# Performance work log

Hardware: AMD Instinct MI355X
Metric: run time of the kernel (lower is better)

The kernel has to match this reference:

```python
import jax, jax.numpy as jnp
import numpy as np

EMBED_DIM = 2048
N_HEADS = 32
N_GROUPS = 8
HEAD_SIZE = EMBED_DIM // N_HEADS  # 64
SCALE = HEAD_SIZE ** -0.5
B, S = 2, 2048


def setup_inputs() -> dict:
    key = jax.random.key(0)
    ks = jax.random.split(key, 7)
    kv_dim = N_GROUPS * HEAD_SIZE
    x = jax.random.normal(ks[0], (B, S, EMBED_DIM), dtype=jnp.float32)
    # Linear weights stored [in, out] (y = x @ W), matching torch nn.Linear math.
    Wq = jax.random.normal(ks[1], (EMBED_DIM, EMBED_DIM), dtype=jnp.float32) * (EMBED_DIM ** -0.5)
    Wk = jax.random.normal(ks[2], (EMBED_DIM, kv_dim), dtype=jnp.float32) * (EMBED_DIM ** -0.5)
    Wv = jax.random.normal(ks[3], (EMBED_DIM, kv_dim), dtype=jnp.float32) * (EMBED_DIM ** -0.5)
    Wo = jax.random.normal(ks[4], (EMBED_DIM, EMBED_DIM), dtype=jnp.float32) * (EMBED_DIM ** -0.5)
    bo = jnp.zeros((EMBED_DIM,), dtype=jnp.float32)
    # causal boolean mask [S, S], broadcast over batch and heads
    mask = jnp.tril(jnp.ones((S, S), dtype=jnp.bool_))
    return {"x": x, "Wq": Wq, "Wk": Wk, "Wv": Wv, "Wo": Wo, "bo": bo, "mask": mask}


def reference(x, Wq, Wk, Wv, Wo, bo, mask):
    B_, S_, E = x.shape
    q = (x @ Wq).reshape(B_, S_, N_HEADS, HEAD_SIZE).transpose(0, 2, 1, 3)   # [B,H,S,D]
    k = (x @ Wk).reshape(B_, S_, N_GROUPS, HEAD_SIZE).transpose(0, 2, 1, 3)  # [B,G,S,D]
    v = (x @ Wv).reshape(B_, S_, N_GROUPS, HEAD_SIZE).transpose(0, 2, 1, 3)
    # GQA: each KV head serves H//G consecutive query heads (matches torch expand+reshape)
    rep = N_HEADS // N_GROUPS
    k = jnp.repeat(k, rep, axis=1)  # [B,H,S,D]
    v = jnp.repeat(v, rep, axis=1)
    scores = SCALE * jnp.einsum("bhqd,bhkd->bhqk", q, k)          # [B,H,S,S]
    scores = jnp.where(mask, scores, -jnp.inf)
    weights = jax.nn.softmax(scores, axis=-1)                      # dropout in eval mode (identity)
    attn = jnp.einsum("bhqk,bhkd->bhqd", weights, v)               # [B,H,S,D]
    attn = attn.transpose(0, 2, 1, 3).reshape(B_, S_, E)
    return attn @ Wo + bo
```

## Files before the change

kernel.cpp:

```cpp
#include <hip/hip_runtime.h>
#include <hip/hip_fp16.h>

#define E_DIM 2048
#define S_LEN 2048
#define NH 32
#define HD 64
#define KV_DIM 512
#define QKV_N 3072
#define M_ROWS 4096
#define QK_SCALE 0.18033688011112042f

typedef __bf16 bf16x8 __attribute__((ext_vector_type(8)));
typedef float f32x4 __attribute__((ext_vector_type(4)));

__device__ __forceinline__ void async_lds16(const __bf16* g, __bf16* l) {
    __builtin_amdgcn_global_load_lds(
        (const __attribute__((address_space(1))) void*)g,
        (__attribute__((address_space(3))) void*)l, 16, 0, 0);
}

#define BAR() asm volatile("s_barrier" ::: "memory")

__global__ void k_convert(const float* __restrict__ x, __bf16* __restrict__ xb, int n) {
    int i = (blockIdx.x * blockDim.x + threadIdx.x) * 4;
    if (i < n) {
        float4 v = *(const float4*)(x + i);
        xb[i + 0] = (__bf16)v.x;
        xb[i + 1] = (__bf16)v.y;
        xb[i + 2] = (__bf16)v.z;
        xb[i + 3] = (__bf16)v.w;
    }
}

__global__ void k_transpose_all(const float* __restrict__ Wq, const float* __restrict__ Wk,
                                const float* __restrict__ Wv, const float* __restrict__ Wo,
                                __bf16* __restrict__ WtAll, __bf16* __restrict__ WoT) {
    const int which = blockIdx.z;
    const float* W;
    __bf16* dst;
    int N;
    float scale = 1.f;
    if (which == 0)      { W = Wq; dst = WtAll;                                    N = E_DIM;  scale = QK_SCALE; }
    else if (which == 1) { W = Wk; dst = WtAll + (size_t)E_DIM * E_DIM;            N = KV_DIM; }
    else if (which == 2) { W = Wv; dst = WtAll + (size_t)(E_DIM + KV_DIM) * E_DIM; N = KV_DIM; }
    else                 { W = Wo; dst = WoT;                                      N = E_DIM;  }
    const int n0 = blockIdx.x * 32;
    if (n0 >= N) return;
    const int k0 = blockIdx.y * 32;
    __shared__ float tile[32][33];
    int tx = threadIdx.x, ty = threadIdx.y;
#pragma unroll
    for (int j = 0; j < 4; ++j)
        tile[ty + j * 8][tx] = W[(size_t)(k0 + ty + j * 8) * N + n0 + tx];
    __syncthreads();
#pragma unroll
    for (int j = 0; j < 4; ++j)
        dst[(size_t)(n0 + ty + j * 8) * E_DIM + k0 + tx] = (__bf16)(tile[tx][ty + j * 8] * scale);
}

#define STG(g, l, bb, hh, kt) do {                                                              \
    async_lds16((g) + (size_t)((hh) * 128) * K + (size_t)(kt) * 64,                             \
                (l) + (bb) * 16384 + (hh) * 8192);                                              \
    async_lds16((g) + (size_t)((hh) * 128 + 64) * K + (size_t)(kt) * 64,                        \
                (l) + (bb) * 16384 + (hh) * 8192 + 4096);                                       \
} while (0)

#define LDA_(p, mq) do {                                                                        \
    _Pragma("unroll") for (int i_ = 0; i_ < 4; ++i_) {                                          \
        const char* rp_ = pAs + (p) * 32768 + ((mq) * 128 + rA + i_ * 16) * 128;                \
        a[i_][0] = *(const bf16x8*)(rp_ + swzk0);                                               \
        a[i_][1] = *(const bf16x8*)(rp_ + swzk1);                                               \
    }                                                                                           \
} while (0)

#define LDB_(p, nq, b) do {                                                                     \
    _Pragma("unroll") for (int j_ = 0; j_ < 2; ++j_) {                                          \
        const char* rp_ = pBs + (p) * 32768 + ((nq) * 128 + rB + j_ * 16) * 128;                \
        b[j_][0] = *(const bf16x8*)(rp_ + swzk0);                                               \
        b[j_][1] = *(const bf16x8*)(rp_ + swzk1);                                               \
    }                                                                                           \
} while (0)

#define MM(mq, nq, b) do {                                                                      \
    __builtin_amdgcn_s_setprio(1);                                                              \
    _Pragma("unroll") for (int i_ = 0; i_ < 4; ++i_)                                            \
    _Pragma("unroll") for (int j_ = 0; j_ < 2; ++j_) {                                          \
        acc[mq][nq][i_][j_] = __builtin_amdgcn_mfma_f32_16x16x32_bf16(                          \
            a[i_][0], b[j_][0], acc[mq][nq][i_][j_], 0, 0, 0);                                  \
        acc[mq][nq][i_][j_] = __builtin_amdgcn_mfma_f32_16x16x32_bf16(                          \
            a[i_][1], b[j_][1], acc[mq][nq][i_][j_], 0, 0, 0);                                  \
    }                                                                                           \
    __builtin_amdgcn_s_setprio(0);                                                              \
} while (0)

#define GROUP(p, kt, S1, S2, WAITSTMT) do {                                                     \
    LDA_(p, 0);                                                                                 \
    LDB_(p, 0, b0);                                                                             \
    if (S1) STG(gA, lA, (p) ^ 1, 1, (kt) + 1);                                                  \
    BAR(); MM(0, 0, b0); BAR();                                                                 \
    LDB_(p, 1, b1);                                                                             \
    if (S2) STG(gA, lA, (p), 0, (kt) + 2);                                                      \
    BAR(); MM(0, 1, b1); BAR();                                                                 \
    LDA_(p, 1);                                                                                 \
    if (S2) STG(gB, lB, (p), 0, (kt) + 2);                                                      \
    BAR(); MM(1, 1, b1); BAR();                                                                 \
    if (S2) STG(gB, lB, (p), 1, (kt) + 2);                                                      \
    WAITSTMT;                                                                                   \
    BAR(); MM(1, 0, b0); BAR();                                                                 \
} while (0)

__global__ __launch_bounds__(512, 2)
void k_gemm8(const __bf16* __restrict__ A, const __bf16* __restrict__ Bt,
             __bf16* __restrict__ C, int M, int N, int K) {
    __shared__ __attribute__((aligned(16))) __bf16 As[2][16384];
    __shared__ __attribute__((aligned(16))) __bf16 Bs[2][16384];
    const int T = K >> 6;
    const int nbx = N >> 8;
    const int bid = blockIdx.x;
    const int swz = (bid & 7) * ((int)gridDim.x >> 3) + (bid >> 3);
    const int m0 = (swz / nbx) << 8;
    const int n0 = (swz % nbx) << 8;

    const int t = threadIdx.x;
    const int lane = t & 63, w = t >> 6;
    const int quad = lane >> 4, l16 = lane & 15;
    const int wr = w >> 2, wc = w & 3;

    const int rbase = w * 8 + (lane >> 3);
    const int cswz = ((lane & 7) ^ (lane >> 3)) * 8;
    const __bf16* gA = A + (size_t)(m0 + rbase) * K + cswz;
    const __bf16* gB = Bt + (size_t)(n0 + rbase) * K + cswz;
    __bf16* lA = &As[0][0] + w * 512;
    __bf16* lB = &Bs[0][0] + w * 512;

    const int swzk0 = ((0 + quad) ^ (l16 & 7)) * 16;
    const int swzk1 = ((4 + quad) ^ (l16 & 7)) * 16;
    const int rA = wr * 64 + l16;
    const int rB = wc * 32 + l16;
    const char* pAs = (const char*)&As[0][0];
    const char* pBs = (const char*)&Bs[0][0];

    f32x4 acc[2][2][4][2] = {};
    bf16x8 a[4][2], b0[2][2], b1[2][2];

    STG(gA, lA, 0, 0, 0); STG(gA, lA, 0, 1, 0);
    STG(gB, lB, 0, 0, 0); STG(gB, lB, 0, 1, 0);
    STG(gA, lA, 1, 0, 1);
    STG(gB, lB, 1, 0, 1); STG(gB, lB, 1, 1, 1);
    asm volatile("s_waitcnt vmcnt(6)" ::: "memory");
    BAR();

    int p = 0;
    for (int kt = 0; kt < T - 2; ++kt) {
        GROUP(p, kt, 1, 1, asm volatile("s_waitcnt vmcnt(6)" ::: "memory"));
        p ^= 1;
    }
    GROUP(p, T - 2, 1, 0, asm volatile("s_waitcnt vmcnt(0)" ::: "memory"));
    p ^= 1;
    GROUP(p, T - 1, 0, 0, (void)0);

#pragma unroll
    for (int mq = 0; mq < 2; ++mq)
#pragma unroll
        for (int nq = 0; nq < 2; ++nq)
#pragma unroll
            for (int i = 0; i < 4; ++i)
#pragma unroll
                for (int j = 0; j < 2; ++j) {
                    const int row = m0 + mq * 128 + wr * 64 + i * 16 + quad * 4;
                    const int col = n0 + nq * 128 + wc * 32 + j * 16 + l16;
#pragma unroll
                    for (int r = 0; r < 4; ++r)
                        C[(size_t)(row + r) * N + col] = (__bf16)acc[mq][nq][i][j][r];
                }
    (void)M;
}

#define STGA_O(bb, kt) do {                                                                     \
    async_lds16(gA + (size_t)(kt) * 64,                  &As[bb][0] + w * 512);                  \
    async_lds16(gA + (size_t)64 * K + (size_t)(kt) * 64, &As[bb][0] + 4096 + w * 512);          \
} while (0)
#define STGB_O(bb, kt, hh) do {                                                                 \
    async_lds16(gB + (size_t)((hh) * 128) * K + (size_t)(kt) * 64,                              \
                &Bs[bb][0] + (hh) * 8192 + w * 512);                                            \
    async_lds16(gB + (size_t)((hh) * 128 + 64) * K + (size_t)(kt) * 64,                         \
                &Bs[bb][0] + (hh) * 8192 + 4096 + w * 512);                                     \
} while (0)

#define LDA_O(p, mq) do {                                                                       \
    _Pragma("unroll") for (int i_ = 0; i_ < 2; ++i_) {                                          \
        const char* rp_ = pAs + (p) * 16384 + ((mq) * 32 + rA + i_ * 16) * 128;                 \
        a[i_][0] = *(const bf16x8*)(rp_ + swzk0);                                               \
        a[i_][1] = *(const bf16x8*)(rp_ + swzk1);                                               \
    }                                                                                           \
} while (0)

#define LDB_O(p, nq, b) do {                                                                    \
    _Pragma("unroll") for (int j_ = 0; j_ < 2; ++j_) {                                          \
        const char* rp_ = pBs + (p) * 32768 + ((nq) * 128 + rB + j_ * 16) * 128;                \
        b[j_][0] = *(const bf16x8*)(rp_ + swzk0);                                               \
        b[j_][1] = *(const bf16x8*)(rp_ + swzk1);                                               \
    }                                                                                           \
} while (0)

#define MM_O(mq, nq, b) do {                                                                    \
    __builtin_amdgcn_s_setprio(1);                                                              \
    _Pragma("unroll") for (int i_ = 0; i_ < 2; ++i_)                                            \
    _Pragma("unroll") for (int j_ = 0; j_ < 2; ++j_) {                                          \
        acc[mq][nq][i_][j_] = __builtin_amdgcn_mfma_f32_16x16x32_bf16(                          \
            a[i_][0], b[j_][0], acc[mq][nq][i_][j_], 0, 0, 0);                                  \
        acc[mq][nq][i_][j_] = __builtin_amdgcn_mfma_f32_16x16x32_bf16(                          \
            a[i_][1], b[j_][1], acc[mq][nq][i_][j_], 0, 0, 0);                                  \
    }                                                                                           \
    __builtin_amdgcn_s_setprio(0);                                                              \
} while (0)

#define GROUP_O(p, kt, S1, S2, WAITSTMT) do {                                                   \
    LDA_O(p, 0);                                                                                \
    LDB_O(p, 0, b0);                                                                            \
    if (S1) STGB_O((p) ^ 1, (kt) + 1, 1);                                                       \
    BAR(); MM_O(0, 0, b0); BAR();                                                               \
    LDB_O(p, 1, b1);                                                                            \
    if (S2) STGB_O(p, (kt) + 2, 0);                                                             \
    BAR(); MM_O(0, 1, b1); BAR();                                                               \
    LDA_O(p, 1);                                                                                \
    BAR(); MM_O(1, 1, b1); BAR();                                                               \
    if (S2) STGA_O(p, (kt) + 2);                                                                \
    WAITSTMT;                                                                                   \
    BAR(); MM_O(1, 0, b0); BAR();                                                               \
} while (0)

__global__ __launch_bounds__(512, 2)
void k_gemm8o(const __bf16* __restrict__ A, const __bf16* __restrict__ Bt,
              float* __restrict__ C, const float* __restrict__ bias,
              int M, int N, int K) {
    __shared__ __attribute__((aligned(16))) __bf16 As[2][8192];
    __shared__ __attribute__((aligned(16))) __bf16 Bs[2][16384];
    const int T = K >> 6;
    const int nbx = N >> 8;
    const int bid = blockIdx.x;
    const int swz = (bid & 7) * ((int)gridDim.x >> 3) + (bid >> 3);
    const int m0 = (swz / nbx) << 7;
    const int n0 = (swz % nbx) << 8;

    const int t = threadIdx.x;
    const int lane = t & 63, w = t >> 6;
    const int quad = lane >> 4, l16 = lane & 15;
    const int wr = w >> 2, wc = w & 3;

    const int rbase = w * 8 + (lane >> 3);
    const int cswz = ((lane & 7) ^ (lane >> 3)) * 8;
    const __bf16* gA = A + (size_t)(m0 + rbase) * K + cswz;
    const __bf16* gB = Bt + (size_t)(n0 + rbase) * K + cswz;

    const int swzk0 = ((0 + quad) ^ (l16 & 7)) * 16;
    const int swzk1 = ((4 + quad) ^ (l16 & 7)) * 16;
    const int rA = wr * 64 + l16;
    const int rB = wc * 32 + l16;
    const char* pAs = (const char*)&As[0][0];
    const char* pBs = (const char*)&Bs[0][0];

    f32x4 acc[2][2][2][2] = {};
    bf16x8 a[2][2], b0[2][2], b1[2][2];

    STGA_O(0, 0); STGB_O(0, 0, 0); STGB_O(0, 0, 1);
    STGB_O(1, 1, 0); STGA_O(1, 1);
    asm volatile("s_waitcnt vmcnt(4)" ::: "memory");
    BAR();

    int p = 0;
    for (int kt = 0; kt < T - 2; ++kt) {
        GROUP_O(p, kt, 1, 1, asm volatile("s_waitcnt vmcnt(4)" ::: "memory"));
        p ^= 1;
    }
    GROUP_O(p, T - 2, 1, 0, asm volatile("s_waitcnt vmcnt(0)" ::: "memory"));
    p ^= 1;
    GROUP_O(p, T - 1, 0, 0, (void)0);

#pragma unroll
    for (int mq = 0; mq < 2; ++mq)
#pragma unroll
        for (int nq = 0; nq < 2; ++nq)
#pragma unroll
            for (int i = 0; i < 2; ++i)
#pragma unroll
                for (int j = 0; j < 2; ++j) {
                    const int row = m0 + wr * 64 + mq * 32 + i * 16 + quad * 4;
                    const int col = n0 + nq * 128 + wc * 32 + j * 16 + l16;
#pragma unroll
                    for (int r = 0; r < 4; ++r)
                        C[(size_t)(row + r) * N + col] = acc[mq][nq][i][j][r] + bias[col];
                }
    (void)M;
}

__global__ __launch_bounds__(256, 3)
void k_attn(const __bf16* __restrict__ qkv, __half* __restrict__ partO,
            float* __restrict__ partL) {
    const int xr = (int)(gridDim.x - 1 - blockIdx.x);
    int qi, c;
    if (xr < 8)       { qi = xr;                  c = 0; }
    else if (xr < 24) { qi = 8 + ((xr - 8) >> 1); c = (xr - 8) & 1; }
    else if (xr < 48) { qi = 16 + (xr - 24) / 3;  c = (xr - 24) % 3; }
    else              { qi = 24 + ((xr - 48) >> 2); c = (xr - 48) & 3; }
    const int q0 = qi * 64;
    const int k_lo = c * 512;
    const int k_hi = min(k_lo + 512, q0 + 64);

    const int gp = blockIdx.y;
    const int g = gp >> 1;
    const int h0 = g * 4 + (gp & 1) * 2;
    const int b = blockIdx.z;
    const int t = threadIdx.x;
    const int lane = t & 63, wave = t >> 6;
    const int quad = lane >> 4, l16 = lane & 15;

    __shared__ __attribute__((aligned(16))) __bf16 Kls[128 * 64];
    __shared__ __attribute__((aligned(16))) __bf16 vT[64][136];
    __shared__ __attribute__((aligned(16))) __bf16 pT[4][2][1024];

    const __bf16* base = qkv + (size_t)b * S_LEN * QKV_N;
    const int qrow = q0 + wave * 16 + l16;

    bf16x8 qf[2][2];
#pragma unroll
    for (int h = 0; h < 2; ++h)
#pragma unroll
        for (int s = 0; s < 2; ++s)
            qf[h][s] = *(const bf16x8*)(base + (size_t)qrow * QKV_N + (h0 + h) * HD + s * 32 + quad * 8);

    f32x4 o[2][4] = {};
    float l_st[2] = {0.f, 0.f};

    const int vkey = lane * 2, vdg = wave * 16;
    const __bf16* vsrc = base + (E_DIM + KV_DIM) + g * HD + vdg;
    const __bf16* ksrc = base + E_DIM + g * HD;

    const int klocal = lane >> 3;
    const int kdblk = (lane & 7) ^ (klocal & 7);
    const __bf16* gk_base = ksrc + (size_t)(wave * 32 + klocal) * QKV_N + kdblk * 8;
    __bf16* lk_base = Kls + wave * 2048;

    auto qk = [&](int m, f32x4* sA, f32x4* sB) {
        __builtin_amdgcn_s_setprio(1);
#pragma unroll
        for (int kt = 0; kt < 4; ++kt) {
            const int kr = m * 64 + kt * 16 + l16;
            const char* kb_ = (const char*)Kls + kr * 128;
            bf16x8 kf0 = *(const bf16x8*)(kb_ + ((quad ^ (kr & 7)) * 16));
            bf16x8 kf1 = *(const bf16x8*)(kb_ + (((4 + quad) ^ (kr & 7)) * 16));
            f32x4 z = {};
            z = __builtin_amdgcn_mfma_f32_16x16x32_bf16(kf0, qf[0][0], z, 0, 0, 0);
            sA[kt] = __builtin_amdgcn_mfma_f32_16x16x32_bf16(kf1, qf[0][1], z, 0, 0, 0);
            f32x4 ww = {};
            ww = __builtin_amdgcn_mfma_f32_16x16x32_bf16(kf0, qf[1][0], ww, 0, 0, 0);
            sB[kt] = __builtin_amdgcn_mfma_f32_16x16x32_bf16(kf1, qf[1][1], ww, 0, 0, 0);
        }
        __builtin_amdgcn_s_setprio(0);
    };

    auto softmax_p = [&](int kb, int h, f32x4* sc) {
        const bool diag = (kb == q0);
        char* prow = (char*)&pT[wave][h][0] + l16 * 128;
        float lsum = 0.f;
#pragma unroll
        for (int kt = 0; kt < 4; ++kt) {
            f32x4 pv_;
#pragma unroll
            for (int r = 0; r < 4; ++r) pv_[r] = exp2f(sc[kt][r]);
            if (diag) {
                const int kbase = kb + kt * 16 + quad * 4;
#pragma unroll
                for (int r = 0; r < 4; ++r)
                    if (kbase + r > qrow) pv_[r] = 0.f;
            }
#pragma unroll
            for (int r = 0; r < 4; ++r) lsum += pv_[r];
            __bf16 pb[4];
#pragma unroll
            for (int r = 0; r < 4; ++r) pb[r] = (__bf16)pv_[r];
            *(uint2*)(prow + ((2 * kt + (quad >> 1)) ^ (l16 & 7)) * 16 + (quad & 1) * 8) =
                *(const uint2*)pb;
        }
        l_st[h] += lsum;
    };

    auto pv = [&](int m) {
        bf16x8 vf[4][2];
        const int koff = m * 64;
#pragma unroll
        for (int cc = 0; cc < 4; ++cc)
#pragma unroll
            for (int kh = 0; kh < 2; ++kh)
                vf[cc][kh] = *(const bf16x8*)&vT[cc * 16 + l16][koff + kh * 32 + quad * 8];
        __builtin_amdgcn_s_setprio(1);
#pragma unroll
        for (int h = 0; h < 2; ++h) {
            const char* prow = (const char*)&pT[wave][h][0] + l16 * 128;
            bf16x8 pf0 = *(const bf16x8*)(prow + ((0 + quad) ^ (l16 & 7)) * 16);
            bf16x8 pf1 = *(const bf16x8*)(prow + ((4 + quad) ^ (l16 & 7)) * 16);
#pragma unroll
            for (int cc = 0; cc < 4; ++cc) {
                o[h][cc] = __builtin_amdgcn_mfma_f32_16x16x32_bf16(vf[cc][0], pf0, o[h][cc], 0, 0, 0);
                o[h][cc] = __builtin_amdgcn_mfma_f32_16x16x32_bf16(vf[cc][1], pf1, o[h][cc], 0, 0, 0);
            }
        }
        __builtin_amdgcn_s_setprio(0);
    };

    for (int kv0 = k_lo; kv0 < k_hi; kv0 += 128) {
#pragma unroll
        for (int i = 0; i < 4; ++i)
            async_lds16(gk_base + (size_t)(kv0 + i * 8) * QKV_N, lk_base + i * 512);

        const __bf16* vp = vsrc + (size_t)(kv0 + vkey) * QKV_N;
        uint4 va0 = *(const uint4*)(vp);
        uint4 va1 = *(const uint4*)(vp + 8);
        uint4 vb0 = *(const uint4*)(vp + QKV_N);
        uint4 vb1 = *(const uint4*)(vp + QKV_N + 8);

        {
            const unsigned short* a0 = (const unsigned short*)&va0;
            const unsigned short* a1 = (const unsigned short*)&va1;
            const unsigned short* b0_ = (const unsigned short*)&vb0;
            const unsigned short* b1_ = (const unsigned short*)&vb1;
#pragma unroll
            for (int j = 0; j < 8; ++j) {
                *(uint32_t*)&vT[vdg + j][vkey] = (uint32_t)a0[j] | ((uint32_t)b0_[j] << 16);
                *(uint32_t*)&vT[vdg + 8 + j][vkey] = (uint32_t)a1[j] | ((uint32_t)b1_[j] << 16);
            }
        }
        __syncthreads();

        f32x4 scA[4], scB[4];
        qk(0, scA, scB);
        softmax_p(kv0, 0, scA);
        softmax_p(kv0, 1, scB);
        pv(0);

        const int kb1 = kv0 + 64;
        if (kb1 < k_hi) {
            qk(1, scA, scB);
            softmax_p(kb1, 0, scA);
            softmax_p(kb1, 1, scB);
            pv(1);
        }
        __syncthreads();
    }

    const size_t blk = ((size_t)b * 16 + gp) * 80 + xr;
    const size_t pb = blk * (2 * 64 * 64);
#pragma unroll
    for (int h = 0; h < 2; ++h) {
        float lt = l_st[h];
        lt += __shfl_xor(lt, 16);
        lt += __shfl_xor(lt, 32);
        const float inv = 1.f / lt;
        __half* prowO = partO + pb + (size_t)(h * 64 + wave * 16 + l16) * 64 + quad * 4;
#pragma unroll
        for (int dt = 0; dt < 4; ++dt) {
            __half ob[4];
#pragma unroll
            for (int r = 0; r < 4; ++r) ob[r] = __float2half(o[h][dt][r] * inv);
            *(uint2*)(prowO + dt * 16) = *(const uint2*)ob;
        }
        if (quad == 0)
            partL[blk * 128 + h * 64 + wave * 16 + l16] = lt;
    }
}

__global__ __launch_bounds__(256, 4)
void k_combine(const __half* __restrict__ partO, const float* __restrict__ partL,
               __bf16* __restrict__ attnb) {
    const int qi = blockIdx.x, gp = blockIdx.y, b = blockIdx.z;
    const int nc = (qi >> 3) + 1;
    int x0;
    if (qi < 8) x0 = qi;
    else if (qi < 16) x0 = 8 + (qi - 8) * 2;
    else if (qi < 24) x0 = 24 + (qi - 16) * 3;
    else x0 = 48 + (qi - 24) * 4;

    const int t = threadIdx.x;
    const int row = t >> 1, half = t & 1;
    const int h = row >> 6, q = row & 63;
    const int d0 = half * 32;
    const size_t gbase = ((size_t)b * 16 + gp) * 80;

    float W = 0.f;
    float acc[32];
#pragma unroll
    for (int i = 0; i < 32; ++i) acc[i] = 0.f;
    for (int cc = 0; cc < nc; ++cc) {
        const float a = partL[(gbase + x0 + cc) * 128 + h * 64 + q];
        W += a;
        const __half* src = partO + (gbase + x0 + cc) * (2 * 64 * 64) + (size_t)(h * 64 + q) * 64 + d0;
#pragma unroll
        for (int i = 0; i < 32; i += 8) {
            uint4 u = *(const uint4*)(src + i);
            const __half* hs = (const __half*)&u;
#pragma unroll
            for (int j = 0; j < 8; ++j) acc[i + j] += a * __half2float(hs[j]);
        }
    }
    const float inv = 1.f / W;
    const int h_abs = (gp >> 1) * 4 + (gp & 1) * 2 + h;
    __bf16* dst = attnb + ((size_t)b * S_LEN + qi * 64 + q) * E_DIM + h_abs * 64 + d0;
#pragma unroll
    for (int i = 0; i < 32; i += 8) {
        __bf16 ob[8];
#pragma unroll
        for (int j = 0; j < 8; ++j) ob[j] = (__bf16)(acc[i + j] * inv);
        *(uint4*)(dst + i) = *(const uint4*)ob;
    }
}

extern "C" void kernel_launch(void* const* d_in, const int* in_sizes, int n_in,
                              void* d_out, int out_size, void* d_ws, size_t ws_size,
                              hipStream_t stream) {
    const float* x  = (const float*)d_in[0];
    const float* Wq = (const float*)d_in[1];
    const float* Wk = (const float*)d_in[2];
    const float* Wv = (const float*)d_in[3];
    const float* Wo = (const float*)d_in[4];
    const float* bo = (const float*)d_in[5];

    __bf16* xb    = (__bf16*)d_ws;
    __bf16* WtAll = xb + (size_t)M_ROWS * E_DIM;
    __bf16* WoT   = WtAll + (size_t)QKV_N * E_DIM;
    __bf16* qkv   = WoT + (size_t)E_DIM * E_DIM;
    __bf16* attnb = qkv + (size_t)M_ROWS * QKV_N;
    __half* partO = (__half*)(attnb + (size_t)M_ROWS * E_DIM);
    float* partL  = (float*)(partO + (size_t)2560 * 2 * 64 * 64);

    k_convert<<<(M_ROWS * E_DIM / 4 + 255) / 256, 256, 0, stream>>>(x, xb, M_ROWS * E_DIM);
    k_transpose_all<<<dim3(64, 64, 4), dim3(32, 8), 0, stream>>>(Wq, Wk, Wv, Wo, WtAll, WoT);

    k_gemm8<<<dim3((M_ROWS / 256) * (QKV_N / 256)), 512, 0, stream>>>(
        xb, WtAll, qkv, M_ROWS, QKV_N, E_DIM);

    k_attn<<<dim3(80, 16, 2), 256, 0, stream>>>(qkv, partO, partL);
    k_combine<<<dim3(32, 16, 2), 256, 0, stream>>>(partO, partL, attnb);

    k_gemm8o<<<dim3((M_ROWS / 128) * (E_DIM / 256)), 512, 0, stream>>>(
        attnb, WoT, (float*)d_out, bo, M_ROWS, E_DIM, E_DIM);
}
```

Baseline: 318.3 us.

## Double-buffer K tiles and prefetch V registers in attention kernel

Result: slower. 331.6 us (+4.2%).

```diff
diff --git a/kernel.cpp b/kernel.cpp
--- a/kernel.cpp
+++ b/kernel.cpp
@@ -294,7 +294,7 @@
     (void)M;
 }
 
-__global__ __launch_bounds__(256, 3)
+__global__ __launch_bounds__(256, 2)
 void k_attn(const __bf16* __restrict__ qkv, __half* __restrict__ partO,
             float* __restrict__ partL) {
     const int xr = (int)(gridDim.x - 1 - blockIdx.x);
@@ -315,7 +315,7 @@
     const int lane = t & 63, wave = t >> 6;
     const int quad = lane >> 4, l16 = lane & 15;
 
-    __shared__ __attribute__((aligned(16))) __bf16 Kls[128 * 64];
+    __shared__ __attribute__((aligned(16))) __bf16 Kls[2][128 * 64];
     __shared__ __attribute__((aligned(16))) __bf16 vT[64][136];
     __shared__ __attribute__((aligned(16))) __bf16 pT[4][2][1024];
 
@@ -339,14 +339,13 @@
     const int klocal = lane >> 3;
     const int kdblk = (lane & 7) ^ (klocal & 7);
     const __bf16* gk_base = ksrc + (size_t)(wave * 32 + klocal) * QKV_N + kdblk * 8;
-    __bf16* lk_base = Kls + wave * 2048;
-
-    auto qk = [&](int m, f32x4* sA, f32x4* sB) {
+
+    auto qk = [&](const char* kls, int m, f32x4* sA, f32x4* sB) {
         __builtin_amdgcn_s_setprio(1);
 #pragma unroll
         for (int kt = 0; kt < 4; ++kt) {
             const int kr = m * 64 + kt * 16 + l16;
-            const char* kb_ = (const char*)Kls + kr * 128;
+            const char* kb_ = kls + kr * 128;
             bf16x8 kf0 = *(const bf16x8*)(kb_ + ((quad ^ (kr & 7)) * 16));
             bf16x8 kf1 = *(const bf16x8*)(kb_ + (((4 + quad) ^ (kr & 7)) * 16));
             f32x4 z = {};
@@ -408,17 +407,20 @@
         __builtin_amdgcn_s_setprio(0);
     };
 
+    int p = 0;
+    uint4 va0, va1, vb0, vb1;
+    {
+#pragma unroll
+        for (int i = 0; i < 4; ++i)
+            async_lds16(gk_base + (size_t)(k_lo + i * 8) * QKV_N, &Kls[0][0] + wave * 2048 + i * 512);
+        const __bf16* vp = vsrc + (size_t)(k_lo + vkey) * QKV_N;
+        va0 = *(const uint4*)(vp);
+        va1 = *(const uint4*)(vp + 8);
+        vb0 = *(const uint4*)(vp + QKV_N);
+        vb1 = *(const uint4*)(vp + QKV_N + 8);
+    }
+
     for (int kv0 = k_lo; kv0 < k_hi; kv0 += 128) {
-#pragma unroll
-        for (int i = 0; i < 4; ++i)
-            async_lds16(gk_base + (size_t)(kv0 + i * 8) * QKV_N, lk_base + i * 512);
-
-        const __bf16* vp = vsrc + (size_t)(kv0 + vkey) * QKV_N;
-        uint4 va0 = *(const uint4*)(vp);
-        uint4 va1 = *(const uint4*)(vp + 8);
-        uint4 vb0 = *(const uint4*)(vp + QKV_N);
-        uint4 vb1 = *(const uint4*)(vp + QKV_N + 8);
-
         {
             const unsigned short* a0 = (const unsigned short*)&va0;
             const unsigned short* a1 = (const unsigned short*)&va1;
@@ -430,22 +432,38 @@
                 *(uint32_t*)&vT[vdg + 8 + j][vkey] = (uint32_t)a1[j] | ((uint32_t)b1_[j] << 16);
             }
         }
-        __syncthreads();
-
+        asm volatile("s_waitcnt vmcnt(0)" ::: "memory");
+        BAR();
+
+        const int nxt = kv0 + 128;
+        if (nxt < k_hi) {
+#pragma unroll
+            for (int i = 0; i < 4; ++i)
+                async_lds16(gk_base + (size_t)(nxt + i * 8) * QKV_N,
+                            &Kls[p ^ 1][0] + wave * 2048 + i * 512);
+            const __bf16* vp = vsrc + (size_t)(nxt + vkey) * QKV_N;
+            va0 = *(const uint4*)(vp);
+            va1 = *(const uint4*)(vp + 8);
+            vb0 = *(const uint4*)(vp + QKV_N);
+            vb1 = *(const uint4*)(vp + QKV_N + 8);
+        }
+
+        const char* kls = (const char*)&Kls[p][0];
         f32x4 scA[4], scB[4];
-        qk(0, scA, scB);
+        qk(kls, 0, scA, scB);
         softmax_p(kv0, 0, scA);
         softmax_p(kv0, 1, scB);
         pv(0);
 
         const int kb1 = kv0 + 64;
         if (kb1 < k_hi) {
-            qk(1, scA, scB);
+            qk(kls, 1, scA, scB);
             softmax_p(kb1, 0, scA);
             softmax_p(kb1, 1, scB);
             pv(1);
         }
-        __syncthreads();
+        BAR();
+        p ^= 1;
     }
 
     const size_t blk = ((size_t)b * 16 + gp) * 80 + xr;
```
